# Kernel tuning notes

Hardware: AMD Instinct MI355X
Metric: run time of the kernel (lower is better)

Reference implementation:

```python
import jax, jax.numpy as jnp
import numpy as np

EPS = 1e-8

def setup_inputs() -> dict:
    key = jax.random.key(0)
    k1, k2 = jax.random.split(key)
    B, D, H, W, K = 32, 256, 64, 64, 64
    X = jax.random.normal(k1, (B, D, H, W), dtype=jnp.float32)
    std1 = 1.0 / float(np.sqrt(K * D))
    codewords = jax.random.uniform(k2, (K, D), dtype=jnp.float32, minval=-std1, maxval=std1)
    return {"X": X, "codewords": codewords}

def reference(X, codewords):
    B, D = X.shape[0], X.shape[1]
    # (B, D, H, W) -> (B, N, D)
    Xf = X.reshape(B, D, -1).transpose(0, 2, 1)
    # pairwise cosine similarity: normalize then matmul -> (B, N, K)
    Xn = Xf / jnp.maximum(jnp.linalg.norm(Xf, axis=-1, keepdims=True), EPS)
    Cn = codewords / jnp.maximum(jnp.linalg.norm(codewords, axis=-1, keepdims=True), EPS)
    L = jnp.einsum('bnd,kd->bnk', Xn, Cn)
    A = jax.nn.softmax(L, axis=2)
    # aggregate: E[b,k,d] = sum_n A[b,n,k] * (Xf[b,n,d] - C[k,d])
    # expressed without materializing the (B,N,K,D) residual tensor:
    E = jnp.einsum('bnk,bnd->bkd', A, Xf) - A.sum(axis=1)[:, :, None] * codewords[None, :, :]
    return E
```

## Files before the change

kernel.cpp:

```cpp
#include <hip/hip_runtime.h>
#include <hip/hip_bf16.h>
#include <math.h>

#define BB 32
#define DD 256
#define NN 4096
#define KK 64
#define EPSV 1e-8f

typedef __attribute__((ext_vector_type(8))) short short8;
typedef __attribute__((ext_vector_type(4))) float f32x4;

__device__ __forceinline__ unsigned int bf16pair(float a, float b) {
    unsigned int ua = __float_as_uint(a);
    unsigned int ub = __float_as_uint(b);
    ua += 0x7fffu + ((ua >> 16) & 1u);
    ub += 0x7fffu + ((ub >> 16) & 1u);
    return (ua >> 16) | (ub & 0xffff0000u);
}
__device__ __forceinline__ unsigned short bf16one(float a) {
    unsigned int ua = __float_as_uint(a);
    ua += 0x7fffu + ((ua >> 16) & 1u);
    return (unsigned short)(ua >> 16);
}

__global__ void k_cnorm(const float* __restrict__ C, float* __restrict__ rcn) {
    int k = threadIdx.x;
    const float4* c4 = (const float4*)(C + k * DD);
    float ss = 0.f;
#pragma unroll 8
    for (int i = 0; i < DD / 4; i++) {
        float4 v = c4[i];
        ss = fmaf(v.x, v.x, ss);
        ss = fmaf(v.y, v.y, ss);
        ss = fmaf(v.z, v.z, ss);
        ss = fmaf(v.w, v.w, ss);
    }
    rcn[k] = 1.f / fmaxf(sqrtf(ss), EPSV);
}

__global__ __launch_bounds__(256) void k_fused(const float* __restrict__ X,
                                               const float* __restrict__ C,
                                               const float* __restrict__ rcn,
                                               float* __restrict__ P,
                                               float* __restrict__ Sp) {
    __shared__ unsigned short cn_s[KK * DD];
    __shared__ unsigned short xnd_s[64 * DD];
    __shared__ unsigned short xdn_s[DD * 64];
    __shared__ unsigned short at_s[KK * 64];
    __shared__ float psum[8 * 64];
    __shared__ float rn_s[64];
    __shared__ float s_red[4 * 64];

    int t = threadIdx.x;
    int b = blockIdx.x >> 4;
    int chunk = blockIdx.x & 15;
    int w = t >> 6;
    int lane = t & 63;
    int c = lane & 15;
    int g = lane >> 4;
    int c7 = c & 7;

#pragma unroll
    for (int i = 0; i < 16; i++) {
        int idx = i * 1024 + t * 4;
        int k = idx >> 8, d = idx & 255;
        float4 v = *(const float4*)(C + idx);
        float r = rcn[k];
        unsigned u0 = bf16pair(v.x * r, v.y * r);
        unsigned u1 = bf16pair(v.z * r, v.w * r);
        int us = k * DD + ((((d >> 3) ^ (k & 7)) << 3) | (d & 7));
        *(unsigned int*)(cn_s + us) = u0;
        *(unsigned int*)(cn_s + us + 2) = u1;
    }

    f32x4 eacc[4][4];
#pragma unroll
    for (int dt = 0; dt < 4; dt++)
#pragma unroll
        for (int kt = 0; kt < 4; kt++) eacc[dt][kt] = (f32x4){0.f, 0.f, 0.f, 0.f};
    float s_acc[4][4];
#pragma unroll
    for (int kt = 0; kt < 4; kt++)
#pragma unroll
        for (int r = 0; r < 4; r++) s_acc[kt][r] = 0.f;

    for (int p = 0; p < 4; p++) {
        int n0 = chunk * 256 + p * 64;
        __syncthreads();

        {
            int i5 = t & 31;
            int dof = t >> 5;
            int n2 = 2 * i5;
            int blk = i5 >> 2;
            const float* xb = X + (size_t)b * (DD * NN) + n0 + n2;
            float ss0 = 0.f, ss1 = 0.f;
#pragma unroll 8
            for (int i = 0; i < 32; i++) {
                int d = i * 8 + dof;
                float2 v = *(const float2*)(xb + (size_t)d * NN);
                ss0 = fmaf(v.x, v.x, ss0);
                ss1 = fmaf(v.y, v.y, ss1);
                unsigned u = bf16pair(v.x, v.y);
                *(unsigned int*)(xdn_s + d * 64 + (((blk ^ (d & 7)) << 3) | (n2 & 7))) = u;
                int db = d >> 3, d7 = d & 7;
                xnd_s[n2 * DD + (((db ^ (n2 & 7)) << 3) | d7)] = (unsigned short)(u & 0xffffu);
                xnd_s[(n2 + 1) * DD + (((db ^ ((n2 + 1) & 7)) << 3) | d7)] = (unsigned short)(u >> 16);
            }
            psum[dof * 64 + n2] = ss0;
            psum[dof * 64 + n2 + 1] = ss1;
        }
        __syncthreads();

        if (t < 64) {
            float ss = 0.f;
#pragma unroll
            for (int j = 0; j < 8; j++) ss += psum[j * 64 + t];
            rn_s[t] = 1.f / fmaxf(sqrtf(ss), EPSV);
        }

        short8 bfr[8];
        {
            const unsigned short* xr = xnd_s + (w * 16 + c) * DD;
#pragma unroll
            for (int ks = 0; ks < 8; ks++)
                bfr[ks] = *(const short8*)(xr + ((((ks << 2) + g) ^ c7) << 3));
        }
        f32x4 lacc[4];
#pragma unroll
        for (int kt = 0; kt < 4; kt++) {
            lacc[kt] = (f32x4){0.f, 0.f, 0.f, 0.f};
            const unsigned short* cr = cn_s + (kt * 16 + c) * DD;
#pragma unroll
            for (int ks = 0; ks < 8; ks++) {
                short8 af = *(const short8*)(cr + ((((ks << 2) + g) ^ c7) << 3));
                lacc[kt] = __builtin_amdgcn_mfma_f32_16x16x32_bf16(af, bfr[ks], lacc[kt], 0, 0, 0);
            }
        }
        __syncthreads();

        {
            float rn = rn_s[w * 16 + c];
            float lv[4][4];
            float m = -1e30f;
#pragma unroll
            for (int kt = 0; kt < 4; kt++)
#pragma unroll
                for (int r = 0; r < 4; r++) {
                    lv[kt][r] = lacc[kt][r] * rn;
                    m = fmaxf(m, lv[kt][r]);
                }
            m = fmaxf(m, __shfl_xor(m, 16));
            m = fmaxf(m, __shfl_xor(m, 32));
            float s = 0.f;
#pragma unroll
            for (int kt = 0; kt < 4; kt++)
#pragma unroll
                for (int r = 0; r < 4; r++) {
                    lv[kt][r] = __expf(lv[kt][r] - m);
                    s += lv[kt][r];
                }
            s += __shfl_xor(s, 16);
            s += __shfl_xor(s, 32);
            float inv = 1.f / s;
            int nn = w * 16 + c;
            int nb = nn >> 3, n7 = nn & 7;
#pragma unroll
            for (int kt = 0; kt < 4; kt++)
#pragma unroll
                for (int r = 0; r < 4; r++) {
                    float a = lv[kt][r] * inv;
                    s_acc[kt][r] += a;
                    int k = kt * 16 + (g << 2) + r;
                    at_s[k * 64 + (((nb ^ (k & 7)) << 3) | n7)] = bf16one(a);
                }
        }
        __syncthreads();

#pragma unroll
        for (int ks2 = 0; ks2 < 2; ks2++) {
            short8 bk[4];
#pragma unroll
            for (int kt = 0; kt < 4; kt++)
                bk[kt] = *(const short8*)(at_s + (kt * 16 + c) * 64 +
                                          ((((ks2 << 2) + g) ^ c7) << 3));
#pragma unroll
            for (int dt = 0; dt < 4; dt++) {
                short8 af = *(const short8*)(xdn_s + (w * 64 + dt * 16 + c) * 64 +
                                             ((((ks2 << 2) + g) ^ c7) << 3));
#pragma unroll
                for (int kt = 0; kt < 4; kt++)
                    eacc[dt][kt] =
                        __builtin_amdgcn_mfma_f32_16x16x32_bf16(af, bk[kt], eacc[dt][kt], 0, 0, 0);
            }
        }
    }

#pragma unroll
    for (int kt = 0; kt < 4; kt++)
#pragma unroll
        for (int r = 0; r < 4; r++) {
            float v = s_acc[kt][r];
            v += __shfl_xor(v, 1);
            v += __shfl_xor(v, 2);
            v += __shfl_xor(v, 4);
            v += __shfl_xor(v, 8);
            if (c == 0) s_red[w * 64 + kt * 16 + (g << 2) + r] = v;
        }
    __syncthreads();
    if (t < 64) Sp[blockIdx.x * 64 + t] = s_red[t] + s_red[64 + t] + s_red[128 + t] + s_red[192 + t];

    float* Pb = P + (size_t)blockIdx.x * (DD * KK);
#pragma unroll
    for (int dt = 0; dt < 4; dt++)
#pragma unroll
        for (int kt = 0; kt < 4; kt++)
#pragma unroll
            for (int r = 0; r < 4; r++) {
                int d = w * 64 + dt * 16 + (g << 2) + r;
                Pb[d * 64 + kt * 16 + c] = eacc[dt][kt][r];
            }
}

__global__ __launch_bounds__(256) void k_fin(const float* __restrict__ P,
                                             const float* __restrict__ Sp,
                                             const float* __restrict__ C,
                                             float* __restrict__ out) {
    int idx = blockIdx.x * 256 + threadIdx.x;
    int b = idx >> 14;
    int r = idx & 16383;
    int d = r >> 6;
    int k = r & 63;
    float e = 0.f, s = 0.f;
    int base = b * 16;
#pragma unroll
    for (int cc = 0; cc < 16; cc++) {
        e += P[(size_t)(base + cc) * (DD * KK) + d * 64 + k];
        s += Sp[(base + cc) * 64 + k];
    }
    out[(size_t)(b * 64 + k) * 256 + d] = e - s * C[k * 256 + d];
}

extern "C" void kernel_launch(void* const* d_in, const int* in_sizes, int n_in,
                              void* d_out, int out_size, void* d_ws, size_t ws_size,
                              hipStream_t stream) {
    const float* X = (const float*)d_in[0];
    const float* C = (const float*)d_in[1];
    float* out = (float*)d_out;
    unsigned char* ws = (unsigned char*)d_ws;

    float* rcn = (float*)(ws);
    float* Sp = (float*)(ws + 256);
    float* P = (float*)(ws + 256 + 512 * KK * 4);

    k_cnorm<<<1, 64, 0, stream>>>(C, rcn);
    k_fused<<<512, 256, 0, stream>>>(X, C, rcn, P, Sp);
    k_fin<<<2048, 256, 0, stream>>>(P, Sp, C, out);
}
```

Baseline: 234.9 us.

## Keep normalized codewords in registers and widen X loads in fused kernel

Drops the separate codeword-norm kernel. Each wave now computes the norm of its own 16 codewords and keeps them in registers as bf16 MFMA operands, which removes the 32KB shared codeword tile and raises occupancy (launch bounds set to 2 blocks per SM). X is loaded with float4 instead of float2 and written to a padded, swizzled n-major shared tile. The work split for the similarity matmul now follows codewords per wave, so the softmax max and sum need cross-wave reductions through shared memory and extra barriers.

```diff
diff --git a/kernel.cpp b/kernel.cpp
--- a/kernel.cpp
+++ b/kernel.cpp
@@ -7,6 +7,7 @@
 #define NN 4096
 #define KK 64
 #define EPSV 1e-8f
+#define XSTR 264
 
 typedef __attribute__((ext_vector_type(8))) short short8;
 typedef __attribute__((ext_vector_type(4))) float f32x4;
@@ -24,54 +25,51 @@
     return (unsigned short)(ua >> 16);
 }
 
-__global__ void k_cnorm(const float* __restrict__ C, float* __restrict__ rcn) {
-    int k = threadIdx.x;
-    const float4* c4 = (const float4*)(C + k * DD);
-    float ss = 0.f;
-#pragma unroll 8
-    for (int i = 0; i < DD / 4; i++) {
-        float4 v = c4[i];
-        ss = fmaf(v.x, v.x, ss);
-        ss = fmaf(v.y, v.y, ss);
-        ss = fmaf(v.z, v.z, ss);
-        ss = fmaf(v.w, v.w, ss);
-    }
-    rcn[k] = 1.f / fmaxf(sqrtf(ss), EPSV);
-}
-
-__global__ __launch_bounds__(256) void k_fused(const float* __restrict__ X,
-                                               const float* __restrict__ C,
-                                               const float* __restrict__ rcn,
-                                               float* __restrict__ P,
-                                               float* __restrict__ Sp) {
-    __shared__ unsigned short cn_s[KK * DD];
-    __shared__ unsigned short xnd_s[64 * DD];
+__global__ __launch_bounds__(256, 2) void k_fused(const float* __restrict__ X,
+                                                  const float* __restrict__ C,
+                                                  float* __restrict__ P,
+                                                  float* __restrict__ Sp) {
+    __shared__ unsigned short xnd_s[64 * XSTR];
     __shared__ unsigned short xdn_s[DD * 64];
-    __shared__ unsigned short at_s[KK * 64];
-    __shared__ float psum[8 * 64];
+    __shared__ unsigned short at_s[KK * 72];
+    __shared__ float red_m[4 * 64];
+    __shared__ float red_s[4 * 64];
     __shared__ float rn_s[64];
-    __shared__ float s_red[4 * 64];
+    float* psum = (float*)at_s;
 
     int t = threadIdx.x;
-    int b = blockIdx.x >> 4;
-    int chunk = blockIdx.x & 15;
-    int w = t >> 6;
-    int lane = t & 63;
-    int c = lane & 15;
-    int g = lane >> 4;
-    int c7 = c & 7;
-
-#pragma unroll
-    for (int i = 0; i < 16; i++) {
-        int idx = i * 1024 + t * 4;
-        int k = idx >> 8, d = idx & 255;
-        float4 v = *(const float4*)(C + idx);
-        float r = rcn[k];
-        unsigned u0 = bf16pair(v.x * r, v.y * r);
-        unsigned u1 = bf16pair(v.z * r, v.w * r);
-        int us = k * DD + ((((d >> 3) ^ (k & 7)) << 3) | (d & 7));
-        *(unsigned int*)(cn_s + us) = u0;
-        *(unsigned int*)(cn_s + us + 2) = u1;
+    int b = blockIdx.x >> 4, chunk = blockIdx.x & 15;
+    int w = t >> 6, lane = t & 63, c = lane & 15, g = lane >> 4;
+    int q = t >> 4;
+    int n4 = c * 4;
+
+    short8 cnf[8];
+    {
+        int k = 16 * w + c;
+        const float* cp = C + k * DD;
+        float4 v0[8], v1[8];
+        float ss = 0.f;
+#pragma unroll
+        for (int ks = 0; ks < 8; ks++) {
+            v0[ks] = *(const float4*)(cp + 32 * ks + 8 * g);
+            v1[ks] = *(const float4*)(cp + 32 * ks + 8 * g + 4);
+            ss = fmaf(v0[ks].x, v0[ks].x, ss); ss = fmaf(v0[ks].y, v0[ks].y, ss);
+            ss = fmaf(v0[ks].z, v0[ks].z, ss); ss = fmaf(v0[ks].w, v0[ks].w, ss);
+            ss = fmaf(v1[ks].x, v1[ks].x, ss); ss = fmaf(v1[ks].y, v1[ks].y, ss);
+            ss = fmaf(v1[ks].z, v1[ks].z, ss); ss = fmaf(v1[ks].w, v1[ks].w, ss);
+        }
+        ss += __shfl_xor(ss, 16);
+        ss += __shfl_xor(ss, 32);
+        float r = 1.f / fmaxf(sqrtf(ss), EPSV);
+#pragma unroll
+        for (int ks = 0; ks < 8; ks++) {
+            uint4 u;
+            u.x = bf16pair(v0[ks].x * r, v0[ks].y * r);
+            u.y = bf16pair(v0[ks].z * r, v0[ks].w * r);
+            u.z = bf16pair(v1[ks].x * r, v1[ks].y * r);
+            u.w = bf16pair(v1[ks].z * r, v1[ks].w * r);
+            cnf[ks] = *(short8*)&u;
+        }
     }
 
     f32x4 eacc[4][4];
@@ -79,102 +77,126 @@
     for (int dt = 0; dt < 4; dt++)
 #pragma unroll
         for (int kt = 0; kt < 4; kt++) eacc[dt][kt] = (f32x4){0.f, 0.f, 0.f, 0.f};
-    float s_acc[4][4];
-#pragma unroll
-    for (int kt = 0; kt < 4; kt++)
-#pragma unroll
-        for (int r = 0; r < 4; r++) s_acc[kt][r] = 0.f;
+    float s_acc[4] = {0.f, 0.f, 0.f, 0.f};
 
     for (int p = 0; p < 4; p++) {
         int n0 = chunk * 256 + p * 64;
         __syncthreads();
 
         {
-            int i5 = t & 31;
-            int dof = t >> 5;
-            int n2 = 2 * i5;
-            int blk = i5 >> 2;
-            const float* xb = X + (size_t)b * (DD * NN) + n0 + n2;
-            float ss0 = 0.f, ss1 = 0.f;
-#pragma unroll 8
-            for (int i = 0; i < 32; i++) {
-                int d = i * 8 + dof;
-                float2 v = *(const float2*)(xb + (size_t)d * NN);
-                ss0 = fmaf(v.x, v.x, ss0);
-                ss1 = fmaf(v.y, v.y, ss1);
-                unsigned u = bf16pair(v.x, v.y);
-                *(unsigned int*)(xdn_s + d * 64 + (((blk ^ (d & 7)) << 3) | (n2 & 7))) = u;
-                int db = d >> 3, d7 = d & 7;
-                xnd_s[n2 * DD + (((db ^ (n2 & 7)) << 3) | d7)] = (unsigned short)(u & 0xffffu);
-                xnd_s[(n2 + 1) * DD + (((db ^ ((n2 + 1) & 7)) << 3) | d7)] = (unsigned short)(u >> 16);
-            }
-            psum[dof * 64 + n2] = ss0;
-            psum[dof * 64 + n2 + 1] = ss1;
+            f32x4 ssn = (f32x4){0.f, 0.f, 0.f, 0.f};
+#pragma unroll
+            for (int i = 0; i < 4; i++) {
+                int dbase = q * 4 + 64 * i;
+                const float* xb = X + ((size_t)b * DD + dbase) * NN + n0 + n4;
+                float4 r0 = *(const float4*)(xb);
+                float4 r1 = *(const float4*)(xb + NN);
+                float4 r2 = *(const float4*)(xb + 2 * NN);
+                float4 r3 = *(const float4*)(xb + 3 * NN);
+                ssn.x = fmaf(r0.x, r0.x, ssn.x); ssn.x = fmaf(r1.x, r1.x, ssn.x);
+                ssn.x = fmaf(r2.x, r2.x, ssn.x); ssn.x = fmaf(r3.x, r3.x, ssn.x);
+                ssn.y = fmaf(r0.y, r0.y, ssn.y); ssn.y = fmaf(r1.y, r1.y, ssn.y);
+                ssn.y = fmaf(r2.y, r2.y, ssn.y); ssn.y = fmaf(r3.y, r3.y, ssn.y);
+                ssn.z = fmaf(r0.z, r0.z, ssn.z); ssn.z = fmaf(r1.z, r1.z, ssn.z);
+                ssn.z = fmaf(r2.z, r2.z, ssn.z); ssn.z = fmaf(r3.z, r3.z, ssn.z);
+                ssn.w = fmaf(r0.w, r0.w, ssn.w); ssn.w = fmaf(r1.w, r1.w, ssn.w);
+                ssn.w = fmaf(r2.w, r2.w, ssn.w); ssn.w = fmaf(r3.w, r3.w, ssn.w);
+                const float4 rr[4] = {r0, r1, r2, r3};
+#pragma unroll
+                for (int j = 0; j < 4; j++) {
+                    int d = dbase + j;
+                    uint2 u;
+                    u.x = bf16pair(rr[j].x, rr[j].y);
+                    u.y = bf16pair(rr[j].z, rr[j].w);
+                    int off = d * 64 + ((((n4 >> 3) ^ (d & 7)) << 3) | (n4 & 7));
+                    *(uint2*)(xdn_s + off) = u;
+                }
+                {
+                    float col0[4] = {r0.x, r1.x, r2.x, r3.x};
+                    float col1[4] = {r0.y, r1.y, r2.y, r3.y};
+                    float col2[4] = {r0.z, r1.z, r2.z, r3.z};
+                    float col3[4] = {r0.w, r1.w, r2.w, r3.w};
+                    const float* cols[4] = {col0, col1, col2, col3};
+#pragma unroll
+                    for (int j = 0; j < 4; j++) {
+                        int n = n4 + j;
+                        const float* cl = cols[j];
+                        uint2 u;
+                        u.x = bf16pair(cl[0], cl[1]);
+                        u.y = bf16pair(cl[2], cl[3]);
+                        int blk = (dbase >> 3) ^ ((n >> 2) & 3);
+                        int off = n * XSTR + (blk << 3) + (dbase & 7);
+                        *(uint2*)(xnd_s + off) = u;
+                    }
+                }
+            }
+            *(f32x4*)(psum + q * 64 + n4) = ssn;
         }
         __syncthreads();
 
         if (t < 64) {
             float ss = 0.f;
 #pragma unroll
-            for (int j = 0; j < 8; j++) ss += psum[j * 64 + t];
+            for (int j = 0; j < 16; j++) ss += psum[j * 64 + t];
             rn_s[t] = 1.f / fmaxf(sqrtf(ss), EPSV);
         }
 
-        short8 bfr[8];
-        {
-            const unsigned short* xr = xnd_s + (w * 16 + c) * DD;
-#pragma unroll
-            for (int ks = 0; ks < 8; ks++)
-                bfr[ks] = *(const short8*)(xr + ((((ks << 2) + g) ^ c7) << 3));
-        }
         f32x4 lacc[4];
 #pragma unroll
-        for (int kt = 0; kt < 4; kt++) {
-            lacc[kt] = (f32x4){0.f, 0.f, 0.f, 0.f};
-            const unsigned short* cr = cn_s + (kt * 16 + c) * DD;
-#pragma unroll
-            for (int ks = 0; ks < 8; ks++) {
-                short8 af = *(const short8*)(cr + ((((ks << 2) + g) ^ c7) << 3));
-                lacc[kt] = __builtin_amdgcn_mfma_f32_16x16x32_bf16(af, bfr[ks], lacc[kt], 0, 0, 0);
-            }
-        }
-        __syncthreads();
-
-        {
-            float rn = rn_s[w * 16 + c];
-            float lv[4][4];
-            float m = -1e30f;
-#pragma unroll
-            for (int kt = 0; kt < 4; kt++)
-#pragma unroll
-                for (int r = 0; r < 4; r++) {
-                    lv[kt][r] = lacc[kt][r] * rn;
-                    m = fmaxf(m, lv[kt][r]);
-                }
-            m = fmaxf(m, __shfl_xor(m, 16));
-            m = fmaxf(m, __shfl_xor(m, 32));
+        for (int nt = 0; nt < 4; nt++) lacc[nt] = (f32x4){0.f, 0.f, 0.f, 0.f};
+#pragma unroll
+        for (int ks = 0; ks < 8; ks++) {
+            short8 af = cnf[ks];
+#pragma unroll
+            for (int nt = 0; nt < 4; nt++) {
+                int n = nt * 16 + c;
+                short8 bf = *(const short8*)(xnd_s + n * XSTR +
+                                             (((4 * ks + g) ^ ((n >> 2) & 3)) << 3));
+                lacc[nt] = __builtin_amdgcn_mfma_f32_16x16x32_bf16(af, bf, lacc[nt], 0, 0, 0);
+            }
+        }
+
+#pragma unroll
+        for (int nt = 0; nt < 4; nt++) {
+            float m0 = fmaxf(fmaxf(lacc[nt][0], lacc[nt][1]), fmaxf(lacc[nt][2], lacc[nt][3]));
+            m0 = fmaxf(m0, __shfl_xor(m0, 16));
+            m0 = fmaxf(m0, __shfl_xor(m0, 32));
+            if (g == 0) red_m[w * 64 + nt * 16 + c] = m0;
+        }
+        __syncthreads();
+
+        float lv[4][4];
+#pragma unroll
+        for (int nt = 0; nt < 4; nt++) {
+            int n = nt * 16 + c;
+            float rn = rn_s[n];
+            float mr = fmaxf(fmaxf(red_m[n], red_m[64 + n]),
+                             fmaxf(red_m[128 + n], red_m[192 + n]));
+            float m = mr * rn;
             float s = 0.f;
 #pragma unroll
-            for (int kt = 0; kt < 4; kt++)
-#pragma unroll
-                for (int r = 0; r < 4; r++) {
-                    lv[kt][r] = __expf(lv[kt][r] - m);
-                    s += lv[kt][r];
-                }
+            for (int r = 0; r < 4; r++) {
+                lv[nt][r] = __expf(lacc[nt][r] * rn - m);
+                s += lv[nt][r];
+            }
             s += __shfl_xor(s, 16);
             s += __shfl_xor(s, 32);
-            float inv = 1.f / s;
-            int nn = w * 16 + c;
-            int nb = nn >> 3, n7 = nn & 7;
-#pragma unroll
-            for (int kt = 0; kt < 4; kt++)
-#pragma unroll
-                for (int r = 0; r < 4; r++) {
-                    float a = lv[kt][r] * inv;
-                    s_acc[kt][r] += a;
-                    int k = kt * 16 + (g << 2) + r;
-                    at_s[k * 64 + (((nb ^ (k & 7)) << 3) | n7)] = bf16one(a);
-                }
+            if (g == 0) red_s[w * 64 + nt * 16 + c] = s;
+        }
+        __syncthreads();
+
+#pragma unroll
+        for (int nt = 0; nt < 4; nt++) {
+            int n = nt * 16 + c;
+            float denom = red_s[n] + red_s[64 + n] + red_s[128 + n] + red_s[192 + n];
+            float inv = 1.f / denom;
+#pragma unroll
+            for (int r = 0; r < 4; r++) {
+                float a = lv[nt][r] * inv;
+                s_acc[r] += a;
+                int k = 16 * w + 4 * g + r;
+                at_s[k * 72 + ((((n >> 3) ^ (k & 7)) << 3) | (n & 7))] = bf16one(a);
+            }
         }
         __syncthreads();
 
@@ -182,13 +204,14 @@
         for (int ks2 = 0; ks2 < 2; ks2++) {
             short8 bk[4];
 #pragma unroll
-            for (int kt = 0; kt < 4; kt++)
-                bk[kt] = *(const short8*)(at_s + (kt * 16 + c) * 64 +
-                                          ((((ks2 << 2) + g) ^ c7) << 3));
+            for (int kt = 0; kt < 4; kt++) {
+                int k = kt * 16 + c;
+                bk[kt] = *(const short8*)(at_s + k * 72 + (((4 * ks2 + g) ^ (k & 7)) << 3));
+            }
 #pragma unroll
             for (int dt = 0; dt < 4; dt++) {
-                short8 af = *(const short8*)(xdn_s + (w * 64 + dt * 16 + c) * 64 +
-                                             ((((ks2 << 2) + g) ^ c7) << 3));
+                int d = w * 64 + dt * 16 + c;
+                short8 af = *(const short8*)(xdn_s + d * 64 + (((4 * ks2 + g) ^ (d & 7)) << 3));
 #pragma unroll
                 for (int kt = 0; kt < 4; kt++)
                     eacc[dt][kt] =
@@ -197,20 +220,6 @@
         }
     }
 
-#pragma unroll
-    for (int kt = 0; kt < 4; kt++)
-#pragma unroll
-        for (int r = 0; r < 4; r++) {
-            float v = s_acc[kt][r];
-            v += __shfl_xor(v, 1);
-            v += __shfl_xor(v, 2);
-            v += __shfl_xor(v, 4);
-            v += __shfl_xor(v, 8);
-            if (c == 0) s_red[w * 64 + kt * 16 + (g << 2) + r] = v;
-        }
-    __syncthreads();
-    if (t < 64) Sp[blockIdx.x * 64 + t] = s_red[t] + s_red[64 + t] + s_red[128 + t] + s_red[192 + t];
-
     float* Pb = P + (size_t)blockIdx.x * (DD * KK);
 #pragma unroll
     for (int dt = 0; dt < 4; dt++)
@@ -218,9 +227,18 @@
         for (int kt = 0; kt < 4; kt++)
 #pragma unroll
             for (int r = 0; r < 4; r++) {
-                int d = w * 64 + dt * 16 + (g << 2) + r;
+                int d = w * 64 + dt * 16 + 4 * g + r;
                 Pb[d * 64 + kt * 16 + c] = eacc[dt][kt][r];
             }
+#pragma unroll
+    for (int r = 0; r < 4; r++) {
+        float v = s_acc[r];
+        v += __shfl_xor(v, 1);
+        v += __shfl_xor(v, 2);
+        v += __shfl_xor(v, 4);
+        v += __shfl_xor(v, 8);
+        if (c == 0) Sp[blockIdx.x * 64 + 16 * w + 4 * g + r] = v;
+    }
 }
 
 __global__ __launch_bounds__(256) void k_fin(const float* __restrict__ P,
@@ -250,11 +268,9 @@
     float* out = (float*)d_out;
     unsigned char* ws = (unsigned char*)d_ws;
 
-    float* rcn = (float*)(ws);
-    float* Sp = (float*)(ws + 256);
-    float* P = (float*)(ws + 256 + 512 * KK * 4);
-
-    k_cnorm<<<1, 64, 0, stream>>>(C, rcn);
-    k_fused<<<512, 256, 0, stream>>>(X, C, rcn, P, Sp);
+    float* Sp = (float*)ws;
+    float* P = (float*)(ws + 131072);
+
+    k_fused<<<512, 256, 0, stream>>>(X, C, P, Sp);
     k_fin<<<2048, 256, 0, stream>>>(P, Sp, C, out);
 }
```

New measurement: 214.7 us. -8.6%, faster.
